# Performance work log

Measured on AMD Instinct MI355X. Metric: run time of the kernel, lower is better.

The kernel has to match this reference:

```python
import jax, jax.numpy as jnp
import numpy as np
from jax import lax

B, N_BASES, C_IN, C_OUT, K, HW = 32, 5, 128, 128, 3, 56

def setup_inputs() -> dict:
    key = jax.random.key(0)
    k1, k2, k3 = jax.random.split(key, 3)
    x = jax.random.normal(k1, (B, C_IN, HW, HW), dtype=jnp.float32)
    weights = jax.random.normal(k2, (N_BASES, C_OUT, C_IN, K, K), dtype=jnp.float32) * 0.05
    scales = jax.random.uniform(k3, (N_BASES,), dtype=jnp.float32)
    return {"x": x, "weights": weights, "scales": scales}

def _binarize(w):
    # per-base: sign(w) * mean(|w|) over the whole weight tensor of that base
    m = jnp.mean(jnp.abs(w), axis=(1, 2, 3, 4), keepdims=True)  # [N,1,1,1,1]
    return jnp.sign(w) * m

def reference(x, weights, scales):
    # torch pads with constant value 1 (not zero) once, then all bases share it
    xp = jnp.pad(x, ((0, 0), (0, 0), (1, 1), (1, 1)), constant_values=1.0)
    wq = _binarize(weights)                              # [N,O,I,K,K]
    wf = wq.reshape(N_BASES * C_OUT, C_IN, K, K)          # fuse bases into one conv
    out = lax.conv_general_dilated(
        xp, wf, window_strides=(1, 1), padding='VALID',
        dimension_numbers=('NCHW', 'OIHW', 'NCHW'))      # [B, N*O, H, W]
    out = out.reshape(B, N_BASES, C_OUT, HW, HW)
    return jnp.einsum('bnohw,n->bohw', out, scales)
```

## Files before the change

kernel.cpp:

```cpp
#include <hip/hip_runtime.h>
#include <stdint.h>

#define N_BASES 5
#define WELEM (128 * 128 * 3 * 3)

typedef __attribute__((ext_vector_type(4))) float f32x4;
typedef __attribute__((ext_vector_type(8))) short bf16x8;

__device__ __forceinline__ unsigned short f2bf(float v) {
  union { float f; uint32_t u; } un;
  un.f = v;
  uint32_t r = un.u + 0x7FFFu + ((un.u >> 16) & 1u);
  return (unsigned short)(r >> 16);
}

__device__ __forceinline__ void glds16(const void* g, void* l) {
  __builtin_amdgcn_global_load_lds(
      (const __attribute__((address_space(1))) void*)g,
      (__attribute__((address_space(3))) void*)l, 16, 0, 0);
}

__global__ __launch_bounds__(256) void prep_fused(
    const float* __restrict__ x, const float* __restrict__ w,
    unsigned short* __restrict__ xp, float* __restrict__ csum_part) {
  int bi = blockIdx.x;
  if (bi >= 1856) {
    int id = bi - 1856;
    int n = id >> 6;
    int chunk = id & 63;
    const f32x4* wb = (const f32x4*)(w + (size_t)n * WELEM + chunk * 2304);
    float s = 0.f;
    for (int i = threadIdx.x; i < 576; i += 256) {
      f32x4 v = wb[i];
      s += fabsf(v.x) + fabsf(v.y) + fabsf(v.z) + fabsf(v.w);
    }
    #pragma unroll
    for (int off = 32; off > 0; off >>= 1) s += __shfl_down(s, off);
    __shared__ float red[4];
    if ((threadIdx.x & 63) == 0) red[threadIdx.x >> 6] = s;
    __syncthreads();
    if (threadIdx.x == 0) csum_part[id] = red[0] + red[1] + red[2] + red[3];
    return;
  }
  int b = bi / 58;
  int hp = bi - b * 58;
  unsigned short* dst = xp + ((size_t)b * 58 + hp) * 58 * 128;
  int gh = hp - 1;
  if ((unsigned)gh >= 56u) {
    uint4 ones = make_uint4(0x3F803F80u, 0x3F803F80u, 0x3F803F80u, 0x3F803F80u);
    for (int i = threadIdx.x; i < 928; i += 256) ((uint4*)dst)[i] = ones;
    return;
  }
  __shared__ unsigned short tile[128][61];
  const float* src = x + ((size_t)b * 128 * 56 + gh) * 56;
  for (int i = threadIdx.x; i < 128 * 14; i += 256) {
    int c = i / 14;
    int k = i - c * 14;
    f32x4 v = *(const f32x4*)(src + (size_t)c * 3136 + k * 4);
    tile[c][1 + 4 * k + 0] = f2bf(v.x);
    tile[c][1 + 4 * k + 1] = f2bf(v.y);
    tile[c][1 + 4 * k + 2] = f2bf(v.z);
    tile[c][1 + 4 * k + 3] = f2bf(v.w);
  }
  if (threadIdx.x < 128) {
    tile[threadIdx.x][0] = 0x3F80;
    tile[threadIdx.x][57] = 0x3F80;
  }
  __syncthreads();
  for (int i = threadIdx.x; i < 928; i += 256) {
    int wp = i >> 4;
    int c8 = i & 15;
    union { uint4 q; unsigned short h[8]; } u;
    #pragma unroll
    for (int j = 0; j < 8; ++j) u.h[j] = tile[c8 * 8 + j][wp];
    *(uint4*)(dst + (size_t)wp * 128 + c8 * 8) = u.q;
  }
}

__global__ __launch_bounds__(256) void binweight_kernel(
    const float* __restrict__ w, const float* __restrict__ csum_part,
    const float* __restrict__ scales, unsigned short* __restrict__ wq) {
  __shared__ float parts[320];
  __shared__ float coef[N_BASES];
  for (int i = threadIdx.x; i < 320; i += 256) parts[i] = csum_part[i];
  __syncthreads();
  if (threadIdx.x < N_BASES) {
    float s = 0.f;
    #pragma unroll 8
    for (int k = 0; k < 64; ++k) s += parts[threadIdx.x * 64 + k];
    coef[threadIdx.x] = scales[threadIdx.x] * s * (1.0f / (float)WELEM);
  }
  __syncthreads();
  int f = blockIdx.x * 256 + threadIdx.x;
  float s = 0.f;
  #pragma unroll
  for (int n = 0; n < N_BASES; ++n) {
    float cn = coef[n];
    float v = w[n * WELEM + f];
    s += (v > 0.f) ? cn : ((v < 0.f) ? -cn : 0.f);
  }
  int o = f / 1152;
  int rem = f - o * 1152;
  int i = rem / 9;
  int t = rem - i * 9;
  int half = i >> 6;
  int c8 = (i >> 3) & 7;
  int e = i & 7;
  wq[(size_t)(t * 2 + half) * 8192 + o * 64 + ((c8 ^ (o & 7)) << 3) + e] = f2bf(s);
}

__global__ __launch_bounds__(256, 2) void conv_kernel(
    const unsigned short* __restrict__ xp, const unsigned short* __restrict__ wq,
    float* __restrict__ out) {
  __shared__ unsigned short patch[27648];
  __shared__ unsigned short btile[8192];

  const int tid = threadIdx.x;
  const int blk = blockIdx.x;
  const int pair = blk & 15;
  const int tileIdx = blk >> 4;
  const int hi = tileIdx >> 2;
  const int wi = tileIdx & 3;
  const int h0 = hi * 4;
  const int w0 = (wi == 3) ? 40 : wi * 16;

  const size_t rowstride = 58 * 128;
  for (int i = tid; i < 3456; i += 256) {
    int img = i / 1728;
    int r = i - img * 1728;
    int sp = r >> 4;
    int c16 = r & 15;
    int ph = sp / 18;
    int pw = sp - ph * 18;
    int b = pair + img * 16;
    const unsigned short* gp = xp + ((size_t)b * 58 + (h0 + ph)) * rowstride +
                               (size_t)(w0 + pw) * 128 + c16 * 8;
    uint4 v = *(const uint4*)gp;
    *(uint4*)&patch[img * 13824 + sp * 128 + ((c16 ^ (sp & 7)) << 3)] = v;
  }

  const int lane = tid & 63;
  const int wave = tid >> 6;
  const int img = wave >> 1;
  const int nh = wave & 1;
  const int l15 = lane & 15;
  const int quad = lane >> 4;

  f32x4 acc[4][4];
  #pragma unroll
  for (int mf = 0; mf < 4; ++mf)
    #pragma unroll
    for (int nf = 0; nf < 4; ++nf) acc[mf][nf] = (f32x4)0.f;

  const unsigned short* pb = &patch[img * 13824];

  #pragma unroll
  for (int t = 0; t < 9; ++t) {
    const int kh = t / 3;
    const int kw = t - kh * 3;
    int sp_mf[4];
    #pragma unroll
    for (int mf = 0; mf < 4; ++mf) sp_mf[mf] = (mf + kh) * 18 + (l15 + kw);
    #pragma unroll
    for (int half = 0; half < 2; ++half) {
      __syncthreads();
      {
        const unsigned short* g =
            wq + (size_t)(t * 2 + half) * 8192 + wave * 2048 + lane * 8;
        unsigned short* l = &btile[wave * 2048];
        #pragma unroll
        for (int j = 0; j < 4; ++j) glds16(g + j * 512, l + j * 512);
      }
      __syncthreads();
      #pragma unroll
      for (int kk = 0; kk < 2; ++kk) {
        const int kb = half * 2 + kk;
        bf16x8 af[4], bf[4];
        #pragma unroll
        for (int mf = 0; mf < 4; ++mf) {
          int sp = sp_mf[mf];
          af[mf] = *(const bf16x8*)&pb[sp * 128 + (((kb * 4 + quad) ^ (sp & 7)) << 3)];
        }
        #pragma unroll
        for (int nf = 0; nf < 4; ++nf) {
          int o = nh * 64 + nf * 16 + l15;
          bf[nf] = *(const bf16x8*)&btile[o * 64 + (((kk * 4 + quad) ^ (o & 7)) << 3)];
        }
        #pragma unroll
        for (int mf = 0; mf < 4; ++mf)
          #pragma unroll
          for (int nf = 0; nf < 4; ++nf)
            acc[mf][nf] = __builtin_amdgcn_mfma_f32_16x16x32_bf16(
                af[mf], bf[nf], acc[mf][nf], 0, 0, 0);
      }
    }
  }

  const int b = pair + img * 16;
  #pragma unroll
  for (int mf = 0; mf < 4; ++mf) {
    int h = h0 + mf;
    #pragma unroll
    for (int nf = 0; nf < 4; ++nf) {
      int o = nh * 64 + nf * 16 + l15;
      float* p = out + (((size_t)b * 128 + o) * 56 + h) * 56 + w0 + quad * 4;
      *(f32x4*)p = acc[mf][nf];
    }
  }
}

extern "C" void kernel_launch(void* const* d_in, const int* in_sizes, int n_in,
                              void* d_out, int out_size, void* d_ws, size_t ws_size,
                              hipStream_t stream) {
  const float* x = (const float*)d_in[0];
  const float* w = (const float*)d_in[1];
  const float* scales = (const float*)d_in[2];
  float* out = (float*)d_out;

  float* csum_part = (float*)d_ws;
  unsigned short* wq = (unsigned short*)((char*)d_ws + 4096);
  unsigned short* xpad = (unsigned short*)((char*)d_ws + 512 * 1024);

  prep_fused<<<1856 + 320, 256, 0, stream>>>(x, w, xpad, csum_part);
  binweight_kernel<<<576, 256, 0, stream>>>(w, csum_part, scales, wq);
  conv_kernel<<<56 * 16, 256, 0, stream>>>(xpad, wq, out);
}
```

Baseline: 153.6 us.

## Triple-buffer weight slices with async LDS DMA and per-slice barriers

```diff
diff --git a/kernel.cpp b/kernel.cpp
--- a/kernel.cpp
+++ b/kernel.cpp
@@ -79,7 +79,7 @@
 
 __global__ __launch_bounds__(256) void binweight_kernel(
     const float* __restrict__ w, const float* __restrict__ csum_part,
-    const float* __restrict__ scales, unsigned short* __restrict__ wq) {
+    const float* __restrict__ scales, unsigned short* __restrict__ wq2) {
   __shared__ float parts[320];
   __shared__ float coef[N_BASES];
   for (int i = threadIdx.x; i < 320; i += 256) parts[i] = csum_part[i];
@@ -103,17 +103,15 @@
   int rem = f - o * 1152;
   int i = rem / 9;
   int t = rem - i * 9;
-  int half = i >> 6;
-  int c8 = (i >> 3) & 7;
-  int e = i & 7;
-  wq[(size_t)(t * 2 + half) * 8192 + o * 64 + ((c8 ^ (o & 7)) << 3) + e] = f2bf(s);
+  int s_idx = t * 4 + (i >> 5);
+  wq2[(size_t)s_idx * 4096 + o * 32 + (i & 31)] = f2bf(s);
 }
 
 __global__ __launch_bounds__(256, 2) void conv_kernel(
-    const unsigned short* __restrict__ xp, const unsigned short* __restrict__ wq,
+    const unsigned short* __restrict__ xp, const unsigned short* __restrict__ wq2,
     float* __restrict__ out) {
   __shared__ unsigned short patch[27648];
-  __shared__ unsigned short btile[8192];
+  __shared__ unsigned short btile[12288];
 
   const int tid = threadIdx.x;
   const int blk = blockIdx.x;
@@ -124,21 +122,6 @@
   const int h0 = hi * 4;
   const int w0 = (wi == 3) ? 40 : wi * 16;
 
-  const size_t rowstride = 58 * 128;
-  for (int i = tid; i < 3456; i += 256) {
-    int img = i / 1728;
-    int r = i - img * 1728;
-    int sp = r >> 4;
-    int c16 = r & 15;
-    int ph = sp / 18;
-    int pw = sp - ph * 18;
-    int b = pair + img * 16;
-    const unsigned short* gp = xp + ((size_t)b * 58 + (h0 + ph)) * rowstride +
-                               (size_t)(w0 + pw) * 128 + c16 * 8;
-    uint4 v = *(const uint4*)gp;
-    *(uint4*)&patch[img * 13824 + sp * 128 + ((c16 ^ (sp & 7)) << 3)] = v;
-  }
-
   const int lane = tid & 63;
   const int wave = tid >> 6;
   const int img = wave >> 1;
@@ -146,6 +129,34 @@
   const int l15 = lane & 15;
   const int quad = lane >> 4;
 
+  const unsigned short* wq_base = wq2 + wave * 1024 + lane * 8;
+  unsigned short* lds_base = &btile[wave * 1024];
+  auto dma = [&](int s) {
+    const unsigned short* g = wq_base + (size_t)s * 4096;
+    unsigned short* l = lds_base + (s % 3) * 4096;
+    glds16(g, l);
+    glds16(g + 512, l + 512);
+  };
+
+  dma(0);
+  dma(1);
+
+  const size_t rowstride = 58 * 128;
+  for (int i = tid; i < 3456; i += 256) {
+    int im = i / 1728;
+    int r = i - im * 1728;
+    int sp = r >> 4;
+    int c16 = r & 15;
+    int ph = sp / 18;
+    int pw = sp - ph * 18;
+    int b = pair + im * 16;
+    const unsigned short* gp = xp + ((size_t)b * 58 + (h0 + ph)) * rowstride +
+                               (size_t)(w0 + pw) * 128 + c16 * 8;
+    uint4 v = *(const uint4*)gp;
+    *(uint4*)&patch[im * 13824 + sp * 128 + ((c16 ^ (sp & 7)) << 3)] = v;
+  }
+  __syncthreads();
+
   f32x4 acc[4][4];
   #pragma unroll
   for (int mf = 0; mf < 4; ++mf)
@@ -153,47 +164,38 @@
     for (int nf = 0; nf < 4; ++nf) acc[mf][nf] = (f32x4)0.f;
 
   const unsigned short* pb = &patch[img * 13824];
-
-  #pragma unroll
-  for (int t = 0; t < 9; ++t) {
+  const unsigned short* bt = &btile[(nh * 64) * 32 + quad * 8];
+
+  #pragma unroll
+  for (int p = 0; p < 36; ++p) {
+    const int t = p >> 2;
+    const int kb = p & 3;
     const int kh = t / 3;
     const int kw = t - kh * 3;
-    int sp_mf[4];
-    #pragma unroll
-    for (int mf = 0; mf < 4; ++mf) sp_mf[mf] = (mf + kh) * 18 + (l15 + kw);
-    #pragma unroll
-    for (int half = 0; half < 2; ++half) {
-      __syncthreads();
-      {
-        const unsigned short* g =
-            wq + (size_t)(t * 2 + half) * 8192 + wave * 2048 + lane * 8;
-        unsigned short* l = &btile[wave * 2048];
-        #pragma unroll
-        for (int j = 0; j < 4; ++j) glds16(g + j * 512, l + j * 512);
-      }
-      __syncthreads();
+
+    if (p < 35)
+      __builtin_amdgcn_s_waitcnt(0x0F72);
+    else
+      __builtin_amdgcn_s_waitcnt(0x0F70);
+    __builtin_amdgcn_s_barrier();
+    if (p + 2 < 36) dma(p + 2);
+
+    bf16x8 af[4], bf[4];
+    #pragma unroll
+    for (int mf = 0; mf < 4; ++mf) {
+      int sp = (mf + kh) * 18 + (l15 + kw);
+      af[mf] = *(const bf16x8*)&pb[sp * 128 + (((kb * 4 + quad) ^ (sp & 7)) << 3)];
+    }
+    const unsigned short* bs = bt + (p % 3) * 4096;
+    #pragma unroll
+    for (int nf = 0; nf < 4; ++nf)
+      bf[nf] = *(const bf16x8*)(bs + (nf * 16 + l15) * 32);
+    #pragma unroll
+    for (int mf = 0; mf < 4; ++mf)
       #pragma unroll
-      for (int kk = 0; kk < 2; ++kk) {
-        const int kb = half * 2 + kk;
-        bf16x8 af[4], bf[4];
-        #pragma unroll
-        for (int mf = 0; mf < 4; ++mf) {
-          int sp = sp_mf[mf];
-          af[mf] = *(const bf16x8*)&pb[sp * 128 + (((kb * 4 + quad) ^ (sp & 7)) << 3)];
-        }
-        #pragma unroll
-        for (int nf = 0; nf < 4; ++nf) {
-          int o = nh * 64 + nf * 16 + l15;
-          bf[nf] = *(const bf16x8*)&btile[o * 64 + (((kk * 4 + quad) ^ (o & 7)) << 3)];
-        }
-        #pragma unroll
-        for (int mf = 0; mf < 4; ++mf)
-          #pragma unroll
-          for (int nf = 0; nf < 4; ++nf)
-            acc[mf][nf] = __builtin_amdgcn_mfma_f32_16x16x32_bf16(
-                af[mf], bf[nf], acc[mf][nf], 0, 0, 0);
-      }
-    }
+      for (int nf = 0; nf < 4; ++nf)
+        acc[mf][nf] = __builtin_amdgcn_mfma_f32_16x16x32_bf16(
+            af[mf], bf[nf], acc[mf][nf], 0, 0, 0);
   }
 
   const int b = pair + img * 16;
@@ -218,10 +220,10 @@
   float* out = (float*)d_out;
 
   float* csum_part = (float*)d_ws;
-  unsigned short* wq = (unsigned short*)((char*)d_ws + 4096);
+  unsigned short* wq2 = (unsigned short*)((char*)d_ws + 4096);
   unsigned short* xpad = (unsigned short*)((char*)d_ws + 512 * 1024);
 
   prep_fused<<<1856 + 320, 256, 0, stream>>>(x, w, xpad, csum_part);
-  binweight_kernel<<<576, 256, 0, stream>>>(w, csum_part, scales, wq);
-  conv_kernel<<<56 * 16, 256, 0, stream>>>(xpad, wq, out);
-}
+  binweight_kernel<<<576, 256, 0, stream>>>(w, csum_part, scales, wq2);
+  conv_kernel<<<56 * 16, 256, 0, stream>>>(xpad, wq2, out);
+}
```

Result: no change. 154.7 us (+0.8%).
